# Kernel tuning notes

Measured on AMD Instinct MI355X. Metric: run time of the kernel, lower is better.

## Reference

```python
import jax, jax.numpy as jnp
import numpy as np
from jax import lax

EPS = 1e-12  # torch F.normalize eps

DIM = 192
HEADS = 8
B, H, W = 4, 256, 256


def setup_inputs() -> dict:
    key = jax.random.key(0)
    k1, k2, k3, k4 = jax.random.split(key, 4)
    x = jax.random.normal(k1, (B, DIM, H, W), dtype=jnp.float32)
    # 1x1 conv weights stored as [out, in] matrices (kernel size 1)
    qkv_w = jax.random.normal(k2, (DIM * 3, DIM), dtype=jnp.float32) * (1.0 / np.sqrt(DIM))
    # depthwise 3x3 conv, groups = 3*DIM -> OIHW with I=1
    dw_w = jax.random.normal(k3, (DIM * 3, 1, 3, 3), dtype=jnp.float32) * (1.0 / 3.0)
    proj_w = jax.random.normal(k4, (DIM, DIM), dtype=jnp.float32) * (1.0 / np.sqrt(DIM))
    temperature = jnp.ones((HEADS, 1, 1), dtype=jnp.float32)
    return {"x": x, "qkv_w": qkv_w, "dw_w": dw_w, "proj_w": proj_w, "temperature": temperature}


def _l2_normalize(t):
    # matches torch F.normalize(dim=-1): x / max(||x||, eps)
    n = jnp.sqrt(jnp.sum(t * t, axis=-1, keepdims=True))
    return t / jnp.maximum(n, EPS)


def reference(x, qkv_w, dw_w, proj_w, temperature):
    b, c, h, w = x.shape
    heads = temperature.shape[0]
    head_dim = c // heads
    hw = h * w
    # 1x1 conv == per-pixel GEMM
    qkv = jnp.einsum('bchw,oc->bohw', x, qkv_w)
    # depthwise 3x3 conv, padding=1
    qkv = lax.conv_general_dilated(
        qkv, dw_w, window_strides=(1, 1), padding='SAME',
        dimension_numbers=('NCHW', 'OIHW', 'NCHW'),
        feature_group_count=c * 3)
    q, k, v = jnp.split(qkv, 3, axis=1)
    q = _l2_normalize(q.reshape(b, heads, head_dim, hw))
    k = _l2_normalize(k.reshape(b, heads, head_dim, hw))
    v = v.reshape(b, heads, head_dim, hw)
    # tiny [head_dim, head_dim] attention matrix per (b, head)
    attn = jnp.einsum('bhdn,bhen->bhde', q, k) * temperature  # (heads,1,1) broadcasts
    attn = jax.nn.softmax(attn, axis=-1)
    out = jnp.einsum('bhde,bhen->bhdn', attn, v).reshape(b, c, h, w)
    return jnp.einsum('bchw,oc->bohw', out, proj_w)
```

## Files before the change

kernel.cpp:

```cpp
#include <hip/hip_runtime.h>
#include <stdint.h>

typedef unsigned short u16;
typedef short s16x8 __attribute__((ext_vector_type(8)));
typedef float f32x4 __attribute__((ext_vector_type(4)));

#define HW 65536
#define CD 192
#define C3 576
#define QB ((size_t)HW * C3)

static __device__ __forceinline__ float bf2f(u16 u) {
    return __uint_as_float(((uint32_t)u) << 16);
}
static __device__ __forceinline__ u16 f2bf(float f) {
    uint32_t x = __float_as_uint(f);
    return (u16)((x + 0x7fffu + ((x >> 16) & 1u)) >> 16);
}

__launch_bounds__(256)
__global__ void k_convert(const float* __restrict__ in, u16* __restrict__ out, int n4)
{
    int i = blockIdx.x * 256 + threadIdx.x;
    if (i >= n4) return;
    float4 v = ((const float4*)in)[i];
    ushort4 o;
    o.x = f2bf(v.x); o.y = f2bf(v.y); o.z = f2bf(v.z); o.w = f2bf(v.w);
    ((ushort4*)out)[i] = o;
}

__launch_bounds__(256, 2)
__global__ void k_qkv(const u16* __restrict__ A, const float* __restrict__ x,
                      u16* __restrict__ O, int b0)
{
    __shared__ __attribute__((aligned(16))) u16 As[192 * 40];
    __shared__ __attribute__((aligned(16))) u16 Xs[128 * 40];
    const int t    = threadIdx.x;
    const int pb   = blockIdx.z;
    const int m0g  = blockIdx.y * 192;
    const int p0   = blockIdx.x * 128;
    const int lane = t & 63, wid = t >> 6;
    const int quad = lane >> 4, l16 = lane & 15;
    const int wm0  = (wid >> 1) * 96, wn0 = (wid & 1) * 64;

    f32x4 acc[6][4];
    #pragma unroll
    for (int i = 0; i < 6; i++)
        #pragma unroll
        for (int j = 0; j < 4; j++) acc[i][j] = f32x4{0.f, 0.f, 0.f, 0.f};

    const float* Xb = x + (size_t)(b0 + pb) * CD * HW;

    for (int kk = 0; kk < 6; kk++) {
        if (kk) __syncthreads();
        #pragma unroll
        for (int i = 0; i < 3; i++) {
            int s = t + i * 256;
            int m = s >> 2, part = s & 3;
            uint4 v = *(const uint4*)(A + (size_t)(m0g + m) * CD + kk * 32 + part * 8);
            *(uint4*)(&As[m * 40 + part * 8]) = v;
        }
        #pragma unroll
        for (int i = 0; i < 4; i++) {
            int s = t + i * 256;
            int c_l = s >> 5, seg = s & 31;
            float4 v = *(const float4*)(Xb + (size_t)(kk * 32 + c_l) * HW + p0 + seg * 4);
            Xs[(seg * 4 + 0) * 40 + c_l] = f2bf(v.x);
            Xs[(seg * 4 + 1) * 40 + c_l] = f2bf(v.y);
            Xs[(seg * 4 + 2) * 40 + c_l] = f2bf(v.z);
            Xs[(seg * 4 + 3) * 40 + c_l] = f2bf(v.w);
        }
        __syncthreads();
        s16x8 af[6], bfr[4];
        #pragma unroll
        for (int i = 0; i < 6; i++)
            af[i] = *(const s16x8*)(&As[(wm0 + i * 16 + l16) * 40 + quad * 8]);
        #pragma unroll
        for (int j = 0; j < 4; j++)
            bfr[j] = *(const s16x8*)(&Xs[(wn0 + j * 16 + l16) * 40 + quad * 8]);
        #pragma unroll
        for (int i = 0; i < 6; i++)
            #pragma unroll
            for (int j = 0; j < 4; j++)
                acc[i][j] = __builtin_amdgcn_mfma_f32_16x16x32_bf16(af[i], bfr[j], acc[i][j], 0, 0, 0);
    }

    u16* Ob = O + QB * pb;
    #pragma unroll
    for (int i = 0; i < 6; i++) {
        const int o = m0g + wm0 + i * 16 + quad * 4;
        #pragma unroll
        for (int j = 0; j < 4; j++) {
            const int p = p0 + wn0 + j * 16 + l16;
            ushort4 v;
            v.x = f2bf(acc[i][j][0]); v.y = f2bf(acc[i][j][1]);
            v.z = f2bf(acc[i][j][2]); v.w = f2bf(acc[i][j][3]);
            *(ushort4*)(Ob + (size_t)p * C3 + o) = v;
        }
    }
}

__launch_bounds__(576)
__global__ void k_dw(const u16* __restrict__ qkv, const float* __restrict__ dww,
                     u16* __restrict__ out)
{
    __shared__ float wlds[72 * 73];
    const int t  = threadIdx.x;
    const int pb = blockIdx.z;
    const int h  = blockIdx.y;
    const int w0 = blockIdx.x * 32;

    for (int i = t; i < 5184; i += 576)
        wlds[(i / 72) * 73 + (i % 72)] = dww[i];

    const int cg    = t % 72;
    const int ps    = t / 72;
    const int wbase = w0 + ps * 4;
    __syncthreads();

    float wr[72];
    #pragma unroll
    for (int k = 0; k < 72; k++) wr[k] = wlds[cg * 73 + k];

    const u16* src = qkv + (size_t)pb * QB + (size_t)cg * 8;
    float acc[4][8];
    #pragma unroll
    for (int i = 0; i < 4; i++)
        #pragma unroll
        for (int j = 0; j < 8; j++) acc[i][j] = 0.f;

    #pragma unroll
    for (int dh = 0; dh < 3; dh++) {
        int gh = h + dh - 1;
        if ((unsigned)gh < 256u) {
            const u16* rsrc = src + (size_t)gh * 256 * C3;
            float v[6][8];
            #pragma unroll
            for (int c = 0; c < 6; c++) {
                int gw = wbase + c - 1;
                uint4 raw = make_uint4(0u, 0u, 0u, 0u);
                if ((unsigned)gw < 256u)
                    raw = *(const uint4*)(rsrc + (size_t)gw * C3);
                const u16* rp = (const u16*)&raw;
                #pragma unroll
                for (int j = 0; j < 8; j++) v[c][j] = bf2f(rp[j]);
            }
            #pragma unroll
            for (int wi = 0; wi < 4; wi++)
                #pragma unroll
                for (int dw = 0; dw < 3; dw++)
                    #pragma unroll
                    for (int j = 0; j < 8; j++)
                        acc[wi][j] += v[wi + dw][j] * wr[j * 9 + dh * 3 + dw];
        }
    }

    u16* dst = out + (size_t)pb * QB + ((size_t)h * 256 + wbase) * C3 + cg * 8;
    #pragma unroll
    for (int wi = 0; wi < 4; wi++) {
        uint4 o;
        o.x = (uint32_t)f2bf(acc[wi][0]) | ((uint32_t)f2bf(acc[wi][1]) << 16);
        o.y = (uint32_t)f2bf(acc[wi][2]) | ((uint32_t)f2bf(acc[wi][3]) << 16);
        o.z = (uint32_t)f2bf(acc[wi][4]) | ((uint32_t)f2bf(acc[wi][5]) << 16);
        o.w = (uint32_t)f2bf(acc[wi][6]) | ((uint32_t)f2bf(acc[wi][7]) << 16);
        *(uint4*)(dst + (size_t)wi * C3) = o;
    }
}

#define GNB    16
#define NCHUNK 16

__launch_bounds__(256, 2)
__global__ void k_gram(const u16* __restrict__ dwt, float* __restrict__ gram, int b0)
{
    __shared__ __attribute__((aligned(16))) u16 S[2][48 * 264];
    const int t    = threadIdx.x;
    const int pb   = blockIdx.z, hh = blockIdx.y, blk = blockIdx.x;
    const int lane = t & 63, wid = t >> 6;
    const int quad = lane >> 4, l16 = lane & 15;
    const u16* src = dwt + (size_t)pb * QB + (size_t)blk * (HW / GNB) * C3;
    const int qcol = hh * 24, kcol = CD + hh * 24;
    const int sp_n0 = (t & 127) * 2;
    const int sp_ph = t >> 7;

    f32x4 acc[6];
    #pragma unroll
    for (int i = 0; i < 6; i++) acc[i] = f32x4{0.f, 0.f, 0.f, 0.f};

    uint4 r0[3], r1[3];

    auto stage_load = [&](int cc) {
        const u16* sp = src + (size_t)(cc * 256 + sp_n0) * C3;
        #pragma unroll
        for (int i = 0; i < 3; i++) {
            int part = i * 2 + sp_ph;
            int col  = part < 3 ? qcol + part * 8 : kcol + (part - 3) * 8;
            r0[i] = *(const uint4*)(sp + col);
            r1[i] = *(const uint4*)(sp + C3 + col);
        }
    };
    auto stage_write = [&](int bb) {
        #pragma unroll
        for (int i = 0; i < 3; i++) {
            int part = i * 2 + sp_ph;
            int dstc = part < 3 ? part * 8 : 24 + (part - 3) * 8;
            const u16* a = (const u16*)&r0[i];
            const u16* b = (const u16*)&r1[i];
            #pragma unroll
            for (int w = 0; w < 8; w++) {
                uint32_t d = (uint32_t)a[w] | ((uint32_t)b[w] << 16);
                *(uint32_t*)&S[bb][(dstc + w) * 264 + sp_n0] = d;
            }
        }
    };

    stage_load(0);
    stage_write(0);
    for (int c = 0; c < NCHUNK; c++) {
        const int bb = c & 1;
        __syncthreads();
        if (c + 1 < NCHUNK) stage_load(c + 1);
        #pragma unroll
        for (int kk = 0; kk < 2; kk++) {
            const int k0 = (wid + kk * 4) * 32 + quad * 8;
            s16x8 f0 = *(const s16x8*)&S[bb][( 0 + l16) * 264 + k0];
            s16x8 f1 = *(const s16x8*)&S[bb][(16 + l16) * 264 + k0];
            s16x8 f2 = *(const s16x8*)&S[bb][(32 + l16) * 264 + k0];
            acc[0] = __builtin_amdgcn_mfma_f32_16x16x32_bf16(f0, f0, acc[0], 0, 0, 0);
            acc[1] = __builtin_amdgcn_mfma_f32_16x16x32_bf16(f0, f1, acc[1], 0, 0, 0);
            acc[2] = __builtin_amdgcn_mfma_f32_16x16x32_bf16(f0, f2, acc[2], 0, 0, 0);
            acc[3] = __builtin_amdgcn_mfma_f32_16x16x32_bf16(f1, f1, acc[3], 0, 0, 0);
            acc[4] = __builtin_amdgcn_mfma_f32_16x16x32_bf16(f1, f2, acc[4], 0, 0, 0);
            acc[5] = __builtin_amdgcn_mfma_f32_16x16x32_bf16(f2, f2, acc[5], 0, 0, 0);
        }
        if (c + 1 < NCHUNK) stage_write(bb ^ 1);
    }

    __syncthreads();
    float* red = (float*)&S[0][0];
    #pragma unroll
    for (int tt = 0; tt < 6; tt++)
        #pragma unroll
        for (int r = 0; r < 4; r++)
            red[(wid * 6 + tt) * 256 + (quad * 4 + r) * 16 + l16] = acc[tt][r];
    __syncthreads();
    const int TIr[6] = {0, 0, 0, 1, 1, 2};
    const int TJr[6] = {0, 1, 2, 1, 2, 2};
    float* gb = gram + ((size_t)(b0 + pb) * 8 + hh) * 2304;
    #pragma unroll
    for (int k = 0; k < 6; k++) {
        float s = red[(0 * 6 + k) * 256 + t] + red[(1 * 6 + k) * 256 + t]
                + red[(2 * 6 + k) * 256 + t] + red[(3 * 6 + k) * 256 + t];
        int row = TIr[k] * 16 + (t >> 4);
        int col = TJr[k] * 16 + (t & 15);
        atomicAdd(&gb[row * 48 + col], s);
    }
}

__global__ void k_softmax(const float* __restrict__ gram, const float* __restrict__ temp,
                          float* __restrict__ attnS, int b0)
{
    const int b = b0 + blockIdx.y, hh = blockIdx.x, t = threadIdx.x;
    const float* G = gram + ((size_t)b * 8 + hh) * 2304;
    __shared__ float ksc[24];
    if (t < 24) ksc[t] = 1.f / fmaxf(sqrtf(G[(24 + t) * 48 + 24 + t]), 1e-12f);
    __syncthreads();
    if (t < 24) {
        const float tp = temp[hh];
        const float qs = 1.f / fmaxf(sqrtf(G[t * 48 + t]), 1e-12f);
        const float* row = G + t * 48 + 24;
        float v[24], m = -1e30f;
        #pragma unroll
        for (int e = 0; e < 24; e++) { v[e] = row[e] * qs * ksc[e] * tp; m = fmaxf(m, v[e]); }
        float ssum = 0.f;
        #pragma unroll
        for (int e = 0; e < 24; e++) { v[e] = expf(v[e] - m); ssum += v[e]; }
        const float inv = 1.f / ssum;
        float* orow = attnS + ((size_t)b * 8 + hh) * 576 + t * 24;
        #pragma unroll
        for (int e = 0; e < 24; e++) orow[e] = v[e] * inv;
    }
}

__launch_bounds__(256)
__global__ void k_meff(const float* __restrict__ attnS, const float* __restrict__ projw,
                       u16* __restrict__ meff, int b0, int total)
{
    int g = blockIdx.x * 256 + threadIdx.x;
    if (g >= total) return;
    int b_l = g / 36864, rem = g % 36864;
    int o = rem / CD, c = rem % CD;
    int hh = c / 24, e = c % 24;
    int b = b0 + b_l;
    const float* Arow = attnS + ((size_t)b * 8 + hh) * 576;
    const float* Prow = projw + o * CD + hh * 24;
    float acc = 0.f;
    #pragma unroll
    for (int d = 0; d < 24; d++) acc += Prow[d] * Arow[d * 24 + e];
    meff[(size_t)b * 36864 + o * CD + c] = f2bf(acc);
}

__launch_bounds__(256, 2)
__global__ void k_gemm2(const u16* __restrict__ A, const u16* __restrict__ X,
                        float* __restrict__ O)
{
    __shared__ __attribute__((aligned(16))) u16 As[192 * 40];
    __shared__ __attribute__((aligned(16))) u16 Xs[128 * 40];
    const int t    = threadIdx.x;
    const int pb   = blockIdx.z;
    const int p0   = blockIdx.x * 128;
    const int lane = t & 63, wid = t >> 6;
    const int quad = lane >> 4, l16 = lane & 15;
    const int wm0  = (wid >> 1) * 96, wn0 = (wid & 1) * 64;

    f32x4 acc[6][4];
    #pragma unroll
    for (int i = 0; i < 6; i++)
        #pragma unroll
        for (int j = 0; j < 4; j++) acc[i][j] = f32x4{0.f, 0.f, 0.f, 0.f};

    const u16* Ab = A + (size_t)36864 * pb;
    const u16* Xb = X + QB * pb;

    for (int kk = 0; kk < 6; kk++) {
        if (kk) __syncthreads();
        #pragma unroll
        for (int i = 0; i < 3; i++) {
            int s = t + i * 256;
            int m = s >> 2, part = s & 3;
            uint4 v = *(const uint4*)(Ab + (size_t)m * CD + kk * 32 + part * 8);
            *(uint4*)(&As[m * 40 + part * 8]) = v;
        }
        #pragma unroll
        for (int i = 0; i < 2; i++) {
            int s = t + i * 256;
            int p = s >> 2, part = s & 3;
            uint4 v = *(const uint4*)(Xb + (size_t)(p0 + p) * C3 + 384 + kk * 32 + part * 8);
            *(uint4*)(&Xs[p * 40 + part * 8]) = v;
        }
        __syncthreads();
        s16x8 af[6], bfr[4];
        #pragma unroll
        for (int i = 0; i < 6; i++)
            af[i] = *(const s16x8*)(&As[(wm0 + i * 16 + l16) * 40 + quad * 8]);
        #pragma unroll
        for (int j = 0; j < 4; j++)
            bfr[j] = *(const s16x8*)(&Xs[(wn0 + j * 16 + l16) * 40 + quad * 8]);
        #pragma unroll
        for (int i = 0; i < 6; i++)
            #pragma unroll
            for (int j = 0; j < 4; j++)
                acc[i][j] = __builtin_amdgcn_mfma_f32_16x16x32_bf16(af[i], bfr[j], acc[i][j], 0, 0, 0);
    }

    float* Ob = O + (size_t)CD * HW * pb;
    #pragma unroll
    for (int i = 0; i < 6; i++) {
        const int o = wm0 + i * 16 + quad * 4;
        #pragma unroll
        for (int j = 0; j < 4; j++) {
            const int p = p0 + wn0 + j * 16 + l16;
            #pragma unroll
            for (int r = 0; r < 4; r++)
                Ob[(size_t)(o + r) * HW + p] = acc[i][j][r];
        }
    }
}

extern "C" void kernel_launch(void* const* d_in, const int* in_sizes, int n_in,
                              void* d_out, int out_size, void* d_ws, size_t ws_size,
                              hipStream_t stream)
{
    (void)out_size;
    const float* x     = (const float*)d_in[0];
    const float* qkvw  = (const float*)d_in[1];
    const float* dww   = (const float*)d_in[2];
    const float* projw = (const float*)d_in[3];
    const float* temp  = (const float*)d_in[4];
    for (int i = 0; i < n_in; i++) {
        switch (in_sizes[i]) {
            case 50331648: x     = (const float*)d_in[i]; break;
            case 110592:   qkvw  = (const float*)d_in[i]; break;
            case 5184:     dww   = (const float*)d_in[i]; break;
            case 36864:    projw = (const float*)d_in[i]; break;
            case 8:        temp  = (const float*)d_in[i]; break;
            default: break;
        }
    }
    float* out = (float*)d_out;
    char* ws = (char*)d_ws;

    const size_t gram_off  = 0;
    const size_t asmx_off  = gram_off + 294912;
    const size_t meff_off  = asmx_off + 73728;
    const size_t qkvwb_off = meff_off + 294912;
    const size_t big_off   = (qkvwb_off + 221184 + 255) & ~(size_t)255;

    int P = 4;
    while (P > 1 && big_off + (size_t)P * 2 * QB * 2 > ws_size) P >>= 1;

    float* gram  = (float*)(ws + gram_off);
    float* attnS = (float*)(ws + asmx_off);
    u16*   meff  = (u16*)(ws + meff_off);
    u16*   qkvwb = (u16*)(ws + qkvwb_off);
    u16*   qkvt  = (u16*)(ws + big_off);
    u16*   dwt   = qkvt + (size_t)P * QB;

    hipMemsetAsync(ws + gram_off, 0, 294912, stream);
    k_convert<<<dim3(108), 256, 0, stream>>>(qkvw, qkvwb, 110592 / 4);

    for (int b0 = 0; b0 < 4; b0 += P) {
        k_qkv<<<dim3(512, 3, P), 256, 0, stream>>>(qkvwb, x, qkvt, b0);
        k_dw<<<dim3(8, 256, P), 576, 0, stream>>>(qkvt, dww, dwt);
        k_gram<<<dim3(GNB, 8, P), 256, 0, stream>>>(dwt, gram, b0);
        k_softmax<<<dim3(8, P), 64, 0, stream>>>(gram, temp, attnS, b0);
        k_meff<<<dim3(P * 144), 256, 0, stream>>>(attnS, projw, meff, b0, P * 36864);
        k_gemm2<<<dim3(512, 1, P), 256, 0, stream>>>(
            meff + (size_t)b0 * 36864, dwt, out + (size_t)b0 * CD * HW);
    }
}
```

Baseline: 921.4 us.

## Restructure depthwise conv as persistent grid-stride kernel with 4-channel cells

The depthwise 3x3 kernel is rewritten. It drops the 576-thread blocks that staged 72 weights per thread through shared memory, and instead uses a fixed grid of 256-thread blocks. Each thread owns 4 channels, loads 36 weights straight from global memory and loops over pixel strips in grid-stride fashion. Border handling now clamps addresses and selects zeros, so loads are never under a branch. The aim is to cut register pressure, raise occupancy and issue all 18 loads unconditionally for better memory-level parallelism. In exchange, loads are narrower (8 bytes instead of 16), and the redundant 6-wide row reads now happen once per 4-channel group, which may add memory traffic.

Result: faster. 822.6 us (-10.7%).

```diff
diff --git a/kernel.cpp b/kernel.cpp
--- a/kernel.cpp
+++ b/kernel.cpp
@@ -100,70 +100,91 @@
     }
 }
 
-__launch_bounds__(576)
+#define DW_NB 2304
+
+__launch_bounds__(256, 4)
 __global__ void k_dw(const u16* __restrict__ qkv, const float* __restrict__ dww,
-                     u16* __restrict__ out)
-{
-    __shared__ float wlds[72 * 73];
-    const int t  = threadIdx.x;
-    const int pb = blockIdx.z;
-    const int h  = blockIdx.y;
-    const int w0 = blockIdx.x * 32;
-
-    for (int i = t; i < 5184; i += 576)
-        wlds[(i / 72) * 73 + (i % 72)] = dww[i];
-
-    const int cg    = t % 72;
-    const int ps    = t / 72;
-    const int wbase = w0 + ps * 4;
-    __syncthreads();
-
-    float wr[72];
-    #pragma unroll
-    for (int k = 0; k < 72; k++) wr[k] = wlds[cg * 73 + k];
-
-    const u16* src = qkv + (size_t)pb * QB + (size_t)cg * 8;
-    float acc[4][8];
-    #pragma unroll
-    for (int i = 0; i < 4; i++)
-        #pragma unroll
-        for (int j = 0; j < 8; j++) acc[i][j] = 0.f;
-
-    #pragma unroll
-    for (int dh = 0; dh < 3; dh++) {
-        int gh = h + dh - 1;
-        if ((unsigned)gh < 256u) {
-            const u16* rsrc = src + (size_t)gh * 256 * C3;
-            float v[6][8];
+                     u16* __restrict__ out, int nbat)
+{
+    const int cell = blockIdx.x * 256 + threadIdx.x;
+    const int slot0 = cell / 144;
+    const int cg    = cell - slot0 * 144;
+    const int c0    = cg * 4;
+
+    float wf[36];
+    #pragma unroll
+    for (int i = 0; i < 9; i++)
+        *(float4*)&wf[i * 4] = *(const float4*)(dww + cg * 36 + i * 4);
+
+    const int iters = 4 * nbat;
+    for (int it = 0; it < iters; it++) {
+        const int s  = slot0 + it * 4096;
+        const int pb = s >> 14;
+        const int p0 = (s & 16383) << 2;
+        const int h  = p0 >> 8;
+        const int w0 = p0 & 255;
+
+        const u16* src = qkv + (size_t)pb * QB + c0;
+
+        int coff[6]; bool cval[6];
+        #pragma unroll
+        for (int c = 0; c < 6; c++) {
+            int gw  = w0 + c - 1;
+            cval[c] = (unsigned)gw < 256u;
+            int gwc = gw < 0 ? 0 : (gw > 255 ? 255 : gw);
+            coff[c] = gwc * C3;
+        }
+
+        uint2 raw[3][6];
+        #pragma unroll
+        for (int dh = 0; dh < 3; dh++) {
+            int gh = h + dh - 1;
+            bool rv = (unsigned)gh < 256u;
+            int ghc = gh < 0 ? 0 : (gh > 255 ? 255 : gh);
+            const u16* rs = src + (size_t)ghc * 256 * C3;
             #pragma unroll
             for (int c = 0; c < 6; c++) {
-                int gw = wbase + c - 1;
-                uint4 raw = make_uint4(0u, 0u, 0u, 0u);
-                if ((unsigned)gw < 256u)
-                    raw = *(const uint4*)(rsrc + (size_t)gw * C3);
-                const u16* rp = (const u16*)&raw;
+                uint2 v = *(const uint2*)(rs + coff[c]);
+                bool ok = rv && cval[c];
+                raw[dh][c].x = ok ? v.x : 0u;
+                raw[dh][c].y = ok ? v.y : 0u;
+            }
+        }
+
+        float acc[4][4];
+        #pragma unroll
+        for (int px = 0; px < 4; px++)
+            #pragma unroll
+            for (int j = 0; j < 4; j++) acc[px][j] = 0.f;
+
+        #pragma unroll
+        for (int dh = 0; dh < 3; dh++) {
+            float v[6][4];
+            #pragma unroll
+            for (int c = 0; c < 6; c++) {
+                const u16* rp = (const u16*)&raw[dh][c];
                 #pragma unroll
-                for (int j = 0; j < 8; j++) v[c][j] = bf2f(rp[j]);
+                for (int j = 0; j < 4; j++) v[c][j] = bf2f(rp[j]);
             }
             #pragma unroll
-            for (int wi = 0; wi < 4; wi++)
+            for (int dw = 0; dw < 3; dw++) {
+                const int k = dh * 3 + dw;
                 #pragma unroll
-                for (int dw = 0; dw < 3; dw++)
+                for (int px = 0; px < 4; px++)
                     #pragma unroll
-                    for (int j = 0; j < 8; j++)
-                        acc[wi][j] += v[wi + dw][j] * wr[j * 9 + dh * 3 + dw];
-        }
-    }
-
-    u16* dst = out + (size_t)pb * QB + ((size_t)h * 256 + wbase) * C3 + cg * 8;
-    #pragma unroll
-    for (int wi = 0; wi < 4; wi++) {
-        uint4 o;
-        o.x = (uint32_t)f2bf(acc[wi][0]) | ((uint32_t)f2bf(acc[wi][1]) << 16);
-        o.y = (uint32_t)f2bf(acc[wi][2]) | ((uint32_t)f2bf(acc[wi][3]) << 16);
-        o.z = (uint32_t)f2bf(acc[wi][4]) | ((uint32_t)f2bf(acc[wi][5]) << 16);
-        o.w = (uint32_t)f2bf(acc[wi][6]) | ((uint32_t)f2bf(acc[wi][7]) << 16);
-        *(uint4*)(dst + (size_t)wi * C3) = o;
+                    for (int j = 0; j < 4; j++)
+                        acc[px][j] += v[px + dw][j] * wf[j * 9 + k];
+            }
+        }
+
+        u16* dst = out + (size_t)pb * QB + (size_t)p0 * C3 + c0;
+        #pragma unroll
+        for (int px = 0; px < 4; px++) {
+            uint2 o;
+            o.x = (uint32_t)f2bf(acc[px][0]) | ((uint32_t)f2bf(acc[px][1]) << 16);
+            o.y = (uint32_t)f2bf(acc[px][2]) | ((uint32_t)f2bf(acc[px][3]) << 16);
+            *(uint2*)(dst + (size_t)px * C3) = o;
+        }
     }
 }
 
@@ -411,7 +432,7 @@
 
     for (int b0 = 0; b0 < 4; b0 += P) {
         k_qkv<<<dim3(512, 3, P), 256, 0, stream>>>(qkvwb, x, qkvt, b0);
-        k_dw<<<dim3(8, 256, P), 576, 0, stream>>>(qkvt, dww, dwt);
+        k_dw<<<dim3(DW_NB), 256, 0, stream>>>(qkvt, dww, dwt, P);
         k_gram<<<dim3(GNB, 8, P), 256, 0, stream>>>(dwt, gram, b0);
         k_softmax<<<dim3(8, P), 64, 0, stream>>>(gram, temp, attnS, b0);
         k_meff<<<dim3(P * 144), 256, 0, stream>>>(attnS, projw, meff, b0, P * 36864);
```
